# Kernel tuning notes

Hardware: AMD Instinct MI355X
Metric: run time of the kernel (lower is better)

Reference implementation:

```python
import jax, jax.numpy as jnp
import numpy as np

CTX = 64       # context_size_samples
HOP = 128      # stft hop
CUT = 129      # filter_length//2 + 1


def conv1d(x, w, b, stride, pad):
    # x: [B, Cin, L], w: [Cout, Cin, K]
    out = jax.lax.conv_general_dilated(
        x, w, window_strides=(stride,), padding=[(pad, pad)],
        dimension_numbers=("NCH", "OIH", "NCH"))
    return out + b[None, :, None]


def setup_inputs() -> dict:
    key = jax.random.key(0)
    ks = jax.random.split(key, 16)
    B = 32768
    s = 0.05  # small init scale to avoid gate/sigmoid saturation
    inp = {
        "x": jax.random.normal(ks[0], (B, 512), jnp.float32),
        "h0": jnp.zeros((B, 128), jnp.float32),
        "c0": jnp.zeros((B, 128), jnp.float32),
        "basis": jax.random.normal(ks[1], (258, 1, 256), jnp.float32) * s,
        "w1": jax.random.normal(ks[2], (128, 129, 3), jnp.float32) * s,
        "b1": jax.random.normal(ks[3], (128,), jnp.float32) * s,
        "w2": jax.random.normal(ks[4], (64, 128, 3), jnp.float32) * s,
        "b2": jax.random.normal(ks[5], (64,), jnp.float32) * s,
        "w3": jax.random.normal(ks[6], (64, 64, 3), jnp.float32) * s,
        "b3": jax.random.normal(ks[7], (64,), jnp.float32) * s,
        "w4": jax.random.normal(ks[8], (128, 64, 3), jnp.float32) * s,
        "b4": jax.random.normal(ks[9], (128,), jnp.float32) * s,
        "w_ih": jax.random.normal(ks[10], (512, 128), jnp.float32) * s,
        "w_hh": jax.random.normal(ks[11], (512, 128), jnp.float32) * s,
        "b_ih": jax.random.normal(ks[12], (512,), jnp.float32) * s,
        "b_hh": jax.random.normal(ks[13], (512,), jnp.float32) * s,
        "dec_w": jax.random.normal(ks[14], (1, 128, 1), jnp.float32) * s,
        "dec_b": jax.random.normal(ks[15], (1,), jnp.float32) * s,
    }
    return inp


def reference(x, h0, c0, basis, w1, b1, w2, b2, w3, b3, w4, b4,
              w_ih, w_hh, b_ih, b_hh, dec_w, dec_b):
    B = x.shape[0]
    # prepend zero context, reflect-pad by 64 (ConvSTFT)
    xc = jnp.concatenate([jnp.zeros((B, CTX), x.dtype), x], axis=1)  # [B,576]
    xp = jnp.pad(xc, ((0, 0), (64, 64)), mode="reflect")[:, None, :]  # [B,1,704]
    ft = jax.lax.conv_general_dilated(
        xp, basis, window_strides=(HOP,), padding=[(0, 0)],
        dimension_numbers=("NCH", "OIH", "NCH"))  # [B,258,4]
    real, imag = ft[:, :CUT, :], ft[:, CUT:, :]
    mag = jnp.sqrt(real * real + imag * imag)  # [B,129,4]
    # encoder: 4 conv+relu blocks
    e = jax.nn.relu(conv1d(mag, w1, b1, 1, 1))   # [B,128,4]
    e = jax.nn.relu(conv1d(e, w2, b2, 2, 1))     # [B,64,2]
    e = jax.nn.relu(conv1d(e, w3, b3, 2, 1))     # [B,64,1]
    e = jax.nn.relu(conv1d(e, w4, b4, 1, 1))     # [B,128,1]
    dec_in = e[:, :, 0]  # [B,128]
    # LSTM cell (gate order i,f,g,o as in the slicing)
    gates = dec_in @ w_ih.T + b_ih + h0 @ w_hh.T + b_hh  # [B,512]
    i, f, g, o = jnp.split(gates, 4, axis=1)
    c1 = jax.nn.sigmoid(f) * c0 + jax.nn.sigmoid(i) * jnp.tanh(g)
    h1 = jax.nn.sigmoid(o) * jnp.tanh(c1)
    # decoder: (eval-mode dropout = identity) -> ReLU -> 1x1 conv -> sigmoid
    out = jax.nn.sigmoid(jax.nn.relu(h1) @ dec_w[0, :, 0] + dec_b[0])  # [B]
    # mean over length-1 dim + squeeze is identity here
    return out, h1, c1
```

## Files before the change

kernel.cpp:

```cpp
#include <hip/hip_runtime.h>

typedef _Float16 f16;
typedef _Float16 f16x8 __attribute__((ext_vector_type(8)));
typedef _Float16 f16x4 __attribute__((ext_vector_type(4)));
typedef float f32x4 __attribute__((ext_vector_type(4)));

#define MFMA16(a, b, c) __builtin_amdgcn_mfma_f32_16x16x32_f16((a), (b), (c), 0, 0, 0)

#define BATCH 32768

#define OFF_GATESA  ((size_t)0)
#define OFF_BF      (OFF_GATESA + 8388608)
#define OFF_W1      (OFF_BF + 139264)
#define OFF_W2      (OFF_W1 + 106496)
#define OFF_W3      (OFF_W2 + 49152)
#define OFF_W4      (OFF_W3 + 24576)
#define OFF_WG      (OFF_W4 + 16384)

__device__ __forceinline__ float sigmoid_(float x) { return 1.f / (1.f + __expf(-x)); }

__global__ __launch_bounds__(256) void prep_kernel(
    const float* __restrict__ basis, const float* __restrict__ w1,
    const float* __restrict__ w2, const float* __restrict__ w3,
    const float* __restrict__ w4, const float* __restrict__ w_ih,
    const float* __restrict__ w_hh, f16* __restrict__ Bf3,
    f16* __restrict__ W1i, f16* __restrict__ W2, f16* __restrict__ W3,
    f16* __restrict__ W4, f16* __restrict__ Wg) {
  int t = blockIdx.x * 256 + threadIdx.x;
  for (int idx = t; idx < 8 * 17 * 512; idx += 16384) {
    int jj = idx & 7;
    int lane = (idx >> 3) & 63;
    int rest = idx >> 9;
    int tt = rest % 17, kb = rest / 17;
    int n = tt * 16 + (lane & 15);
    int k = kb * 32 + (lane >> 4) * 8 + jj;
    Bf3[idx] = (f16)((n < 258) ? basis[n * 256 + k] : 0.f);
  }
  for (int idx = t; idx < 13 * 128 * 32; idx += 16384) {
    int kb = idx / 4096, rest = idx - kb * 4096;
    int n = rest >> 5, kk = rest & 31;
    int k = kb * 32 + kk;
    int tap = k / 136, i = k - tap * 136;
    float v = (tap < 3 && i < 129) ? w1[(n * 129 + i) * 3 + tap] : 0.f;
    W1i[idx] = (f16)v;
  }
  for (int idx = t; idx < 64 * 384; idx += 16384) {
    int n = idx / 384, k = idx - n * 384;
    int tap = k >> 7, i = k & 127;
    W2[idx] = (f16)w2[(n * 128 + i) * 3 + tap];
  }
  for (int idx = t; idx < 64 * 192; idx += 16384) {
    int n = idx / 192, k = idx - n * 192;
    int tap = k >> 6, i = k & 63;
    W3[idx] = (f16)w3[(n * 64 + i) * 3 + tap];
  }
  for (int idx = t; idx < 128 * 64; idx += 16384) {
    int n = idx >> 6, i = idx & 63;
    W4[idx] = (f16)w4[(n * 64 + i) * 3 + 1];
  }
  for (int idx = t; idx < 512 * 256; idx += 16384) {
    int n = idx >> 8, k = idx & 255;
    Wg[idx] = (f16)((k < 128) ? w_ih[n * 128 + k] : w_hh[n * 128 + (k - 128)]);
  }
}

__global__ __launch_bounds__(512, 4) void fused_kernel(
    const float* __restrict__ x, const f16* __restrict__ Bf3,
    const f16* __restrict__ W1i, const float* __restrict__ b1,
    const f16* __restrict__ W2, const float* __restrict__ b2,
    const f16* __restrict__ W3, const float* __restrict__ b3,
    const f16* __restrict__ W4, const float* __restrict__ b4,
    f16* __restrict__ gatesA) {
  __shared__ __align__(16) char smem[51968];
  f16* SF = (f16*)smem;
  float* imPatch = (float*)(smem + 49664);
#define XP(bl, j) ((bl)*712 + (j))
#define E1(bl, s, c) ((bl)*648 + (s)*128 + (c))
#define E3(bl, c) ((bl)*72 + (c))
#define MG(bl, j) (11392 + (bl)*840 + (j))
#define E2(bl, s, c) (11392 + (bl)*200 + (s)*64 + (c))

  int tid = threadIdx.x;
  int lane = tid & 63, wv = tid >> 6;
  int l15 = lane & 15, quad = lane >> 4;
  int b0 = blockIdx.x * 16;
  f32x4 zero4 = {0.f, 0.f, 0.f, 0.f};

  for (int idx = tid; idx < 16 * 176; idx += 512) {
    int bl = idx / 176, g = idx - bl * 176;
    int b = b0 + bl;
    f16x4 o;
    if (g < 32) {
      float v0 = (g == 0) ? x[(size_t)b * 512] : 0.f;
      o = (f16x4){(f16)v0, (f16)0.f, (f16)0.f, (f16)0.f};
    } else if (g < 160) {
      const float4 v = *(const float4*)(x + (size_t)b * 512 + 4 * g - 128);
      o = (f16x4){(f16)v.x, (f16)v.y, (f16)v.z, (f16)v.w};
    } else {
      int j0 = 4 * g;
      const float* xb = x + (size_t)b * 512;
      o = (f16x4){(f16)xb[1150 - j0], (f16)xb[1149 - j0], (f16)xb[1148 - j0],
                  (f16)xb[1147 - j0]};
    }
    *(f16x4*)&SF[XP(bl, 4 * g)] = o;
  }
  {
    f16x8 z8 = {};
    for (int idx = tid; idx < 16 * 105; idx += 512) {
      int bl = idx / 105, g = idx - bl * 105;
      *(f16x8*)&SF[MG(bl, g * 8)] = z8;
    }
  }
  __syncthreads();

  {
    const f16* Bl = Bf3 + lane * 8;

    if (wv == 0) {
      f32x4 acc4[4] = {zero4, zero4, zero4, zero4};
      for (int kb = 0; kb < 8; kb++) {
        f16x8 bc4 = *(const f16x8*)(Bl + (size_t)kb * 17 * 512 + 16 * 512);
#pragma unroll
        for (int mt = 0; mt < 4; mt++) {
          f16x8 a = *(const f16x8*)&SF[XP(l15, mt * 128 + kb * 32 + quad * 8)];
          acc4[mt] = MFMA16(a, bc4, acc4[mt]);
        }
      }
      if (l15 < 2) {
        float* dst = imPatch + (l15 == 0 ? 7 : 8) * 64;
#pragma unroll
        for (int mt = 0; mt < 4; mt++)
#pragma unroll
          for (int r = 0; r < 4; r++)
            dst[mt * 16 + quad * 4 + r] = acc4[mt][r];
      }
    }

    int t0 = wv, t1 = wv + 8;
    f32x4 acc0[4], acc1v[4];
#pragma unroll
    for (int mt = 0; mt < 4; mt++) {
      acc0[mt] = zero4;
      acc1v[mt] = zero4;
    }

    for (int kb = 0; kb < 8; kb++) {
      const f16* Bk = Bl + (size_t)kb * 17 * 512;
      f16x8 bc0 = *(const f16x8*)(Bk + t0 * 512);
      f16x8 bc1 = *(const f16x8*)(Bk + t1 * 512);
#pragma unroll
      for (int mt = 0; mt < 4; mt++) {
        f16x8 a = *(const f16x8*)&SF[XP(l15, mt * 128 + kb * 32 + quad * 8)];
        acc0[mt] = MFMA16(a, bc0, acc0[mt]);
        acc1v[mt] = MFMA16(a, bc1, acc1v[mt]);
      }
    }

    if (wv >= 1 && l15 == 0) {
#pragma unroll
      for (int mt = 0; mt < 4; mt++)
#pragma unroll
        for (int r = 0; r < 4; r++)
          imPatch[(wv - 1) * 64 + mt * 16 + quad * 4 + r] = acc1v[mt][r];
    }
    __syncthreads();

#pragma unroll
    for (int mt = 0; mt < 4; mt++)
#pragma unroll
      for (int r = 0; r < 4; r++) {
        int bl = quad * 4 + r;
        int orow = MG(bl, (mt + 1) * 136);
        int row = mt * 16 + quad * 4 + r;
        {
          float re = acc0[mt][r];
          float imA = __shfl(acc1v[mt][r], (quad << 4) | ((l15 + 1) & 15), 64);
          float im = (l15 == 15) ? imPatch[wv * 64 + row] : imA;
          SF[orow + 16 * wv + l15] = (f16)sqrtf(re * re + im * im);
        }
        if (wv == 0 && l15 == 0) {
          float re8 = acc1v[mt][r];
          float im8 = imPatch[8 * 64 + row];
          SF[orow + 128] = (f16)sqrtf(re8 * re8 + im8 * im8);
        }
      }
  }
  __syncthreads();

  {
    f16x8 z8 = {};
    for (int idx = tid; idx < 16 * 16; idx += 512) {
      int bl = idx >> 4, g = idx & 15;
      *(f16x8*)&SF[E1(bl, 0, g * 8)] = z8;
    }
    f32x4 acc1[4];
#pragma unroll
    for (int p = 0; p < 4; p++) acc1[p] = zero4;
    const f16* bbase = W1i + (wv * 16 + l15) * 32 + quad * 8;
    f16x8 bc0 = *(const f16x8*)(bbase);
    for (int kb = 0; kb < 13; kb++) {
      f16x8 bn0;
      if (kb < 12) bn0 = *(const f16x8*)(bbase + (kb + 1) * 4096);
      f16x8 a[4];
#pragma unroll
      for (int p = 0; p < 4; p++)
        a[p] = *(const f16x8*)&SF[MG(l15, p * 136 + kb * 32 + quad * 8)];
#pragma unroll
      for (int p = 0; p < 4; p++) acc1[p] = MFMA16(a[p], bc0, acc1[p]);
      if (kb < 12) bc0 = bn0;
    }
    float bias = b1[wv * 16 + l15];
#pragma unroll
    for (int p = 0; p < 4; p++)
#pragma unroll
      for (int r = 0; r < 4; r++) {
        int bl = quad * 4 + r;
        SF[E1(bl, p + 1, wv * 16 + l15)] =
            (f16)fmaxf(acc1[p][r] + bias, 0.f);
      }
  }
  __syncthreads();

  {
    int wr = wv & 1, wc = wv >> 1;
    {
      f16x8 z8 = {};
      for (int idx = tid; idx < 16 * 8; idx += 512) {
        int bl = idx >> 3, g = idx & 7;
        *(f16x8*)&SF[E2(bl, 0, g * 8)] = z8;
      }
    }
    f32x4 acc2 = zero4;
    const f16* bbase = W2 + (size_t)(wc * 16 + l15) * 384 + quad * 8;
    f16x8 bc0 = *(const f16x8*)(bbase);
    for (int kb = 0; kb < 12; kb++) {
      f16x8 bn0;
      if (kb < 11) bn0 = *(const f16x8*)(bbase + (kb + 1) * 32);
      f16x8 a = *(const f16x8*)&SF[E1(l15, wr * 2, kb * 32 + quad * 8)];
      acc2 = MFMA16(a, bc0, acc2);
      if (kb < 11) bc0 = bn0;
    }
    float bias = b2[wc * 16 + l15];
#pragma unroll
    for (int r = 0; r < 4; r++) {
      int bl = quad * 4 + r;
      SF[E2(bl, wr + 1, wc * 16 + l15)] = (f16)fmaxf(acc2[r] + bias, 0.f);
    }
  }
  __syncthreads();

  if (wv < 4) {
    f32x4 acc3 = zero4;
    const f16* bbase = W3 + (size_t)(wv * 16 + l15) * 192 + quad * 8;
    for (int kb = 0; kb < 6; kb++) {
      f16x8 a = *(const f16x8*)&SF[E2(l15, 0, kb * 32 + quad * 8)];
      f16x8 bf = *(const f16x8*)(bbase + kb * 32);
      acc3 = MFMA16(a, bf, acc3);
    }
    float bias = b3[wv * 16 + l15];
#pragma unroll
    for (int r = 0; r < 4; r++) {
      int bl = quad * 4 + r;
      SF[E3(bl, wv * 16 + l15)] = (f16)fmaxf(acc3[r] + bias, 0.f);
    }
  }
  __syncthreads();

  {
    f32x4 acc4a = zero4;
    const f16* bbase = W4 + (size_t)(wv * 16 + l15) * 64 + quad * 8;
    for (int kb = 0; kb < 2; kb++) {
      f16x8 a = *(const f16x8*)&SF[E3(l15, kb * 32 + quad * 8)];
      f16x8 bf0 = *(const f16x8*)(bbase + kb * 32);
      acc4a = MFMA16(a, bf0, acc4a);
    }
    float bias = b4[wv * 16 + l15];
#pragma unroll
    for (int r = 0; r < 4; r++) {
      int bl = quad * 4 + r;
      gatesA[(size_t)(b0 + bl) * 128 + wv * 16 + l15] =
          (f16)fmaxf(acc4a[r] + bias, 0.f);
    }
  }
#undef XP
#undef MG
#undef E1
#undef E2
#undef E3
}

__global__ __launch_bounds__(512, 2) void gates_kernel(
    const f16* __restrict__ gatesA, const float* __restrict__ h0,
    const f16* __restrict__ Wg, const float* __restrict__ b_ih,
    const float* __restrict__ b_hh, const float* __restrict__ c0,
    const float* __restrict__ dec_w, const float* __restrict__ dec_b,
    float* __restrict__ out) {
  __shared__ float part[4][64];
  int tid = threadIdx.x;
  int lane = tid & 63, wv = tid >> 6;
  int wc = wv & 3;
  int wm = wv >> 2;
  int l15 = lane & 15, quad = lane >> 4;
  int b0 = blockIdx.x * 64;
  f32x4 zero4 = {0.f, 0.f, 0.f, 0.f};

  float* out_h1 = out + BATCH;
  float* out_c1 = out + BATCH + (size_t)BATCH * 128;

  f32x4 acc[2][8];
#pragma unroll
  for (int m = 0; m < 2; m++)
#pragma unroll
    for (int j = 0; j < 8; j++) acc[m][j] = zero4;

  const f16* aptr[2];
  const float* hptr[2];
#pragma unroll
  for (int m = 0; m < 2; m++) {
    int mt = wm * 2 + m;
    aptr[m] = gatesA + (size_t)(b0 + mt * 16 + l15) * 128 + quad * 8;
    hptr[m] = h0 + (size_t)(b0 + mt * 16 + l15) * 128 + quad * 8;
  }

  const f16* bptrs[8];
#pragma unroll
  for (int q = 0; q < 4; q++)
#pragma unroll
    for (int u = 0; u < 2; u++)
      bptrs[q * 2 + u] =
          Wg + (size_t)(q * 128 + wc * 32 + u * 16 + l15) * 256 + quad * 8;

#pragma unroll
  for (int k0 = 0; k0 < 256; k0 += 32) {
    f16x8 a[2];
    if (k0 < 128) {
#pragma unroll
      for (int m = 0; m < 2; m++) a[m] = *(const f16x8*)(aptr[m] + k0);
    } else {
#pragma unroll
      for (int m = 0; m < 2; m++) {
        const float* hp = hptr[m] + (k0 - 128);
        float4 v0 = *(const float4*)hp;
        float4 v1 = *(const float4*)(hp + 4);
        a[m] = (f16x8){(f16)v0.x, (f16)v0.y, (f16)v0.z, (f16)v0.w,
                       (f16)v1.x, (f16)v1.y, (f16)v1.z, (f16)v1.w};
      }
    }
#pragma unroll
    for (int j = 0; j < 8; j++) {
      f16x8 bf = *(const f16x8*)(bptrs[j] + k0);
#pragma unroll
      for (int m = 0; m < 2; m++) acc[m][j] = MFMA16(a[m], bf, acc[m][j]);
    }
  }

  float bias[8], dw[2];
#pragma unroll
  for (int q = 0; q < 4; q++)
#pragma unroll
    for (int u = 0; u < 2; u++) {
      int n = q * 128 + wc * 32 + u * 16 + l15;
      bias[q * 2 + u] = b_ih[n] + b_hh[n];
    }
#pragma unroll
  for (int u = 0; u < 2; u++) dw[u] = dec_w[wc * 32 + u * 16 + l15];

#pragma unroll
  for (int m = 0; m < 2; m++)
#pragma unroll
    for (int r = 0; r < 4; r++) {
      int bl = (wm * 2 + m) * 16 + quad * 4 + r;
      int b = b0 + bl;
      float p = 0.f;
#pragma unroll
      for (int u = 0; u < 2; u++) {
        int c = wc * 32 + u * 16 + l15;
        float iv = acc[m][0 + u][r] + bias[0 + u];
        float fv = acc[m][2 + u][r] + bias[2 + u];
        float gv = acc[m][4 + u][r] + bias[4 + u];
        float ov = acc[m][6 + u][r] + bias[6 + u];
        float c0v = c0[(size_t)b * 128 + c];
        float c1 = sigmoid_(fv) * c0v + sigmoid_(iv) * tanhf(gv);
        float h1 = sigmoid_(ov) * tanhf(c1);
        out_h1[(size_t)b * 128 + c] = h1;
        out_c1[(size_t)b * 128 + c] = c1;
        p += fmaxf(h1, 0.f) * dw[u];
      }
      p += __shfl_xor(p, 1);
      p += __shfl_xor(p, 2);
      p += __shfl_xor(p, 4);
      p += __shfl_xor(p, 8);
      if (l15 == 0) part[wc][bl] = p;
    }
  __syncthreads();
  if (tid < 64) {
    float s = part[0][tid] + part[1][tid] + part[2][tid] + part[3][tid] +
              dec_b[0];
    out[b0 + tid] = 1.f / (1.f + __expf(-s));
  }
}

extern "C" void kernel_launch(void* const* d_in, const int* in_sizes, int n_in,
                              void* d_out, int out_size, void* d_ws,
                              size_t ws_size, hipStream_t stream) {
  const float* x = (const float*)d_in[0];
  const float* h0 = (const float*)d_in[1];
  const float* c0 = (const float*)d_in[2];
  const float* basis = (const float*)d_in[3];
  const float* w1 = (const float*)d_in[4];
  const float* b1 = (const float*)d_in[5];
  const float* w2 = (const float*)d_in[6];
  const float* b2 = (const float*)d_in[7];
  const float* w3 = (const float*)d_in[8];
  const float* b3 = (const float*)d_in[9];
  const float* w4 = (const float*)d_in[10];
  const float* b4 = (const float*)d_in[11];
  const float* w_ih = (const float*)d_in[12];
  const float* w_hh = (const float*)d_in[13];
  const float* b_ih = (const float*)d_in[14];
  const float* b_hh = (const float*)d_in[15];
  const float* dec_w = (const float*)d_in[16];
  const float* dec_b = (const float*)d_in[17];

  char* ws = (char*)d_ws;
  f16* gatesA = (f16*)(ws + OFF_GATESA);
  f16* Bf3 = (f16*)(ws + OFF_BF);
  f16* W1i = (f16*)(ws + OFF_W1);
  f16* W2 = (f16*)(ws + OFF_W2);
  f16* W3 = (f16*)(ws + OFF_W3);
  f16* W4 = (f16*)(ws + OFF_W4);
  f16* Wg = (f16*)(ws + OFF_WG);

  prep_kernel<<<64, 256, 0, stream>>>(basis, w1, w2, w3, w4, w_ih, w_hh, Bf3,
                                      W1i, W2, W3, W4, Wg);
  fused_kernel<<<2048, 512, 0, stream>>>(x, Bf3, W1i, b1, W2, b2, W3, b3, W4,
                                         b4, gatesA);
  gates_kernel<<<512, 512, 0, stream>>>(gatesA, h0, Wg, b_ih, b_hh, c0, dec_w,
                                        dec_b, (float*)d_out);
}
```

Before: 310.9 us.

## Double fused kernel block to 1024 threads, splitting STFT and conv1 rows across waves

The fused encoder kernel now launches 1024-thread blocks (16 waves) instead of 512. The STFT and first-conv stages split their M-tiles (frames) between two wave halves, so each wave keeps two accumulator tiles instead of four. Later small stages run only on the first 8 or 4 waves. The unused reflect-padding tail of the input staging is no longer loaded. The aim is more latency hiding and less per-wave register pressure, at the cost of fewer MFMAs per loaded B fragment and more idle waves in the tail stages.

Measured after the change: 299.7 us. 3.6% less time.

```diff
diff --git a/kernel.cpp b/kernel.cpp
--- a/kernel.cpp
+++ b/kernel.cpp
@@ -64,7 +64,7 @@
   }
 }
 
-__global__ __launch_bounds__(512, 4) void fused_kernel(
+__global__ __launch_bounds__(1024, 8) void fused_kernel(
     const float* __restrict__ x, const f16* __restrict__ Bf3,
     const f16* __restrict__ W1i, const float* __restrict__ b1,
     const f16* __restrict__ W2, const float* __restrict__ b2,
@@ -86,27 +86,22 @@
   int b0 = blockIdx.x * 16;
   f32x4 zero4 = {0.f, 0.f, 0.f, 0.f};
 
-  for (int idx = tid; idx < 16 * 176; idx += 512) {
-    int bl = idx / 176, g = idx - bl * 176;
+  for (int idx = tid; idx < 16 * 160; idx += 1024) {
+    int bl = idx / 160, g = idx - bl * 160;
     int b = b0 + bl;
     f16x4 o;
     if (g < 32) {
       float v0 = (g == 0) ? x[(size_t)b * 512] : 0.f;
       o = (f16x4){(f16)v0, (f16)0.f, (f16)0.f, (f16)0.f};
-    } else if (g < 160) {
+    } else {
       const float4 v = *(const float4*)(x + (size_t)b * 512 + 4 * g - 128);
       o = (f16x4){(f16)v.x, (f16)v.y, (f16)v.z, (f16)v.w};
-    } else {
-      int j0 = 4 * g;
-      const float* xb = x + (size_t)b * 512;
-      o = (f16x4){(f16)xb[1150 - j0], (f16)xb[1149 - j0], (f16)xb[1148 - j0],
-                  (f16)xb[1147 - j0]};
     }
     *(f16x4*)&SF[XP(bl, 4 * g)] = o;
   }
   {
     f16x8 z8 = {};
-    for (int idx = tid; idx < 16 * 105; idx += 512) {
+    for (int idx = tid; idx < 16 * 105; idx += 1024) {
       int bl = idx / 105, g = idx - bl * 105;
       *(f16x8*)&SF[MG(bl, g * 8)] = z8;
     }
@@ -114,72 +109,76 @@
   __syncthreads();
 
   {
+    int tp = wv & 7, mh = wv >> 3;
     const f16* Bl = Bf3 + lane * 8;
 
-    if (wv == 0) {
-      f32x4 acc4[4] = {zero4, zero4, zero4, zero4};
+    if (tp == 0) {
+      f32x4 acc4[2] = {zero4, zero4};
       for (int kb = 0; kb < 8; kb++) {
         f16x8 bc4 = *(const f16x8*)(Bl + (size_t)kb * 17 * 512 + 16 * 512);
 #pragma unroll
-        for (int mt = 0; mt < 4; mt++) {
+        for (int m = 0; m < 2; m++) {
+          int mt = mh * 2 + m;
           f16x8 a = *(const f16x8*)&SF[XP(l15, mt * 128 + kb * 32 + quad * 8)];
-          acc4[mt] = MFMA16(a, bc4, acc4[mt]);
+          acc4[m] = MFMA16(a, bc4, acc4[m]);
         }
       }
       if (l15 < 2) {
         float* dst = imPatch + (l15 == 0 ? 7 : 8) * 64;
 #pragma unroll
-        for (int mt = 0; mt < 4; mt++)
+        for (int m = 0; m < 2; m++)
 #pragma unroll
           for (int r = 0; r < 4; r++)
-            dst[mt * 16 + quad * 4 + r] = acc4[mt][r];
-      }
-    }
-
-    int t0 = wv, t1 = wv + 8;
-    f32x4 acc0[4], acc1v[4];
-#pragma unroll
-    for (int mt = 0; mt < 4; mt++) {
-      acc0[mt] = zero4;
-      acc1v[mt] = zero4;
+            dst[(mh * 2 + m) * 16 + quad * 4 + r] = acc4[m][r];
+      }
+    }
+
+    f32x4 acc0[2], acc1v[2];
+#pragma unroll
+    for (int m = 0; m < 2; m++) {
+      acc0[m] = zero4;
+      acc1v[m] = zero4;
     }
 
     for (int kb = 0; kb < 8; kb++) {
       const f16* Bk = Bl + (size_t)kb * 17 * 512;
-      f16x8 bc0 = *(const f16x8*)(Bk + t0 * 512);
-      f16x8 bc1 = *(const f16x8*)(Bk + t1 * 512);
-#pragma unroll
-      for (int mt = 0; mt < 4; mt++) {
+      f16x8 bc0 = *(const f16x8*)(Bk + tp * 512);
+      f16x8 bc1 = *(const f16x8*)(Bk + (tp + 8) * 512);
+#pragma unroll
+      for (int m = 0; m < 2; m++) {
+        int mt = mh * 2 + m;
         f16x8 a = *(const f16x8*)&SF[XP(l15, mt * 128 + kb * 32 + quad * 8)];
-        acc0[mt] = MFMA16(a, bc0, acc0[mt]);
-        acc1v[mt] = MFMA16(a, bc1, acc1v[mt]);
-      }
-    }
-
-    if (wv >= 1 && l15 == 0) {
-#pragma unroll
-      for (int mt = 0; mt < 4; mt++)
+        acc0[m] = MFMA16(a, bc0, acc0[m]);
+        acc1v[m] = MFMA16(a, bc1, acc1v[m]);
+      }
+    }
+
+    if (tp >= 1 && l15 == 0) {
+#pragma unroll
+      for (int m = 0; m < 2; m++)
 #pragma unroll
         for (int r = 0; r < 4; r++)
-          imPatch[(wv - 1) * 64 + mt * 16 + quad * 4 + r] = acc1v[mt][r];
+          imPatch[(tp - 1) * 64 + (mh * 2 + m) * 16 + quad * 4 + r] =
+              acc1v[m][r];
     }
     __syncthreads();
 
 #pragma unroll
-    for (int mt = 0; mt < 4; mt++)
+    for (int m = 0; m < 2; m++)
 #pragma unroll
       for (int r = 0; r < 4; r++) {
+        int mt = mh * 2 + m;
         int bl = quad * 4 + r;
         int orow = MG(bl, (mt + 1) * 136);
         int row = mt * 16 + quad * 4 + r;
         {
-          float re = acc0[mt][r];
-          float imA = __shfl(acc1v[mt][r], (quad << 4) | ((l15 + 1) & 15), 64);
-          float im = (l15 == 15) ? imPatch[wv * 64 + row] : imA;
-          SF[orow + 16 * wv + l15] = (f16)sqrtf(re * re + im * im);
+          float re = acc0[m][r];
+          float imA = __shfl(acc1v[m][r], (quad << 4) | ((l15 + 1) & 15), 64);
+          float im = (l15 == 15) ? imPatch[tp * 64 + row] : imA;
+          SF[orow + 16 * tp + l15] = (f16)sqrtf(re * re + im * im);
         }
-        if (wv == 0 && l15 == 0) {
-          float re8 = acc1v[mt][r];
+        if (tp == 0 && l15 == 0) {
+          float re8 = acc1v[m][r];
           float im8 = imPatch[8 * 64 + row];
           SF[orow + 128] = (f16)sqrtf(re8 * re8 + im8 * im8);
         }
@@ -189,62 +188,63 @@
 
   {
     f16x8 z8 = {};
-    for (int idx = tid; idx < 16 * 16; idx += 512) {
+    for (int idx = tid; idx < 16 * 16; idx += 1024) {
       int bl = idx >> 4, g = idx & 15;
       *(f16x8*)&SF[E1(bl, 0, g * 8)] = z8;
     }
-    f32x4 acc1[4];
-#pragma unroll
-    for (int p = 0; p < 4; p++) acc1[p] = zero4;
-    const f16* bbase = W1i + (wv * 16 + l15) * 32 + quad * 8;
+    int nt = wv & 7, ph = wv >> 3;
+    f32x4 acc1[2] = {zero4, zero4};
+    const f16* bbase = W1i + (nt * 16 + l15) * 32 + quad * 8;
     f16x8 bc0 = *(const f16x8*)(bbase);
     for (int kb = 0; kb < 13; kb++) {
       f16x8 bn0;
       if (kb < 12) bn0 = *(const f16x8*)(bbase + (kb + 1) * 4096);
-      f16x8 a[4];
-#pragma unroll
-      for (int p = 0; p < 4; p++)
-        a[p] = *(const f16x8*)&SF[MG(l15, p * 136 + kb * 32 + quad * 8)];
-#pragma unroll
-      for (int p = 0; p < 4; p++) acc1[p] = MFMA16(a[p], bc0, acc1[p]);
+#pragma unroll
+      for (int pi = 0; pi < 2; pi++) {
+        int p = ph * 2 + pi;
+        f16x8 a = *(const f16x8*)&SF[MG(l15, p * 136 + kb * 32 + quad * 8)];
+        acc1[pi] = MFMA16(a, bc0, acc1[pi]);
+      }
       if (kb < 12) bc0 = bn0;
     }
-    float bias = b1[wv * 16 + l15];
-#pragma unroll
-    for (int p = 0; p < 4; p++)
+    float bias = b1[nt * 16 + l15];
+#pragma unroll
+    for (int pi = 0; pi < 2; pi++)
 #pragma unroll
       for (int r = 0; r < 4; r++) {
         int bl = quad * 4 + r;
-        SF[E1(bl, p + 1, wv * 16 + l15)] =
-            (f16)fmaxf(acc1[p][r] + bias, 0.f);
+        SF[E1(bl, ph * 2 + pi + 1, nt * 16 + l15)] =
+            (f16)fmaxf(acc1[pi][r] + bias, 0.f);
       }
   }
   __syncthreads();
 
   {
-    int wr = wv & 1, wc = wv >> 1;
     {
       f16x8 z8 = {};
-      for (int idx = tid; idx < 16 * 8; idx += 512) {
+      for (int idx = tid; idx < 16 * 8; idx += 1024) {
         int bl = idx >> 3, g = idx & 7;
         *(f16x8*)&SF[E2(bl, 0, g * 8)] = z8;
       }
     }
-    f32x4 acc2 = zero4;
-    const f16* bbase = W2 + (size_t)(wc * 16 + l15) * 384 + quad * 8;
-    f16x8 bc0 = *(const f16x8*)(bbase);
-    for (int kb = 0; kb < 12; kb++) {
-      f16x8 bn0;
-      if (kb < 11) bn0 = *(const f16x8*)(bbase + (kb + 1) * 32);
-      f16x8 a = *(const f16x8*)&SF[E1(l15, wr * 2, kb * 32 + quad * 8)];
-      acc2 = MFMA16(a, bc0, acc2);
-      if (kb < 11) bc0 = bn0;
-    }
-    float bias = b2[wc * 16 + l15];
-#pragma unroll
-    for (int r = 0; r < 4; r++) {
-      int bl = quad * 4 + r;
-      SF[E2(bl, wr + 1, wc * 16 + l15)] = (f16)fmaxf(acc2[r] + bias, 0.f);
+    if (wv < 8) {
+      int wr = wv & 1, wc = wv >> 1;
+      f32x4 acc2 = zero4;
+      const f16* bbase = W2 + (size_t)(wc * 16 + l15) * 384 + quad * 8;
+      f16x8 bc0 = *(const f16x8*)(bbase);
+      for (int kb = 0; kb < 12; kb++) {
+        f16x8 bn0;
+        if (kb < 11) bn0 = *(const f16x8*)(bbase + (kb + 1) * 32);
+        f16x8 a = *(const f16x8*)&SF[E1(l15, wr * 2, kb * 32 + quad * 8)];
+        acc2 = MFMA16(a, bc0, acc2);
+        if (kb < 11) bc0 = bn0;
+      }
+      float bias = b2[wc * 16 + l15];
+#pragma unroll
+      for (int r = 0; r < 4; r++) {
+        int bl = quad * 4 + r;
+        SF[E2(bl, wr + 1, wc * 16 + l15)] = (f16)fmaxf(acc2[r] + bias, 0.f);
+      }
     }
   }
   __syncthreads();
@@ -266,7 +266,7 @@
   }
   __syncthreads();
 
-  {
+  if (wv < 8) {
     f32x4 acc4a = zero4;
     const f16* bbase = W4 + (size_t)(wv * 16 + l15) * 64 + quad * 8;
     for (int kb = 0; kb < 2; kb++) {
@@ -433,8 +433,8 @@
 
   prep_kernel<<<64, 256, 0, stream>>>(basis, w1, w2, w3, w4, w_ih, w_hh, Bf3,
                                       W1i, W2, W3, W4, Wg);
-  fused_kernel<<<2048, 512, 0, stream>>>(x, Bf3, W1i, b1, W2, b2, W3, b3, W4,
-                                         b4, gatesA);
+  fused_kernel<<<2048, 1024, 0, stream>>>(x, Bf3, W1i, b1, W2, b2, W3, b3, W4,
+                                          b4, gatesA);
   gates_kernel<<<512, 512, 0, stream>>>(gatesA, h0, Wg, b_ih, b_hh, c0, dec_w,
                                         dec_b, (float*)d_out);
 }
```
